# Kernel optimization log

Measured on AMD Instinct MI355X. Metric: run time of the kernel, lower is better.

The kernel has to match this reference:

```python
import jax, jax.numpy as jnp
import numpy as np

B = 1024
E = 512
NUM_HEADS = 8
EPS = 1e-5  # torch LayerNorm default


def _mha(x, w_qkv, b_qkv, w_o, b_o):
    """torch nn.MultiheadAttention (batch_first, self-attn, no dropout).
    x: [N, S, E]; w_qkv: [3E, E]; w_o: [E, E]."""
    N, S, Ex = x.shape
    H = NUM_HEADS
    D = Ex // H
    qkv = x @ w_qkv.T + b_qkv                      # [N, S, 3E]
    q, k, v = jnp.split(qkv, 3, axis=-1)
    q = q.reshape(N, S, H, D).transpose(0, 2, 1, 3)  # [N, H, S, D]
    k = k.reshape(N, S, H, D).transpose(0, 2, 1, 3)
    v = v.reshape(N, S, H, D).transpose(0, 2, 1, 3)
    scores = jnp.einsum('nhqd,nhkd->nhqk', q, k) * (D ** -0.5)
    attn = jax.nn.softmax(scores, axis=-1)
    out = jnp.einsum('nhqk,nhkd->nhqd', attn, v)
    out = out.transpose(0, 2, 1, 3).reshape(N, S, Ex)
    return out @ w_o.T + b_o


def _box_perm(g):
    """Permute 9x9 grid so each 3x3 box becomes a contiguous row of 9.
    This permutation is its own inverse. g: [B, 9, 9, E]."""
    Bx = g.shape[0]
    return (g.reshape(Bx, 3, 3, 3, 3, E)
             .transpose(0, 1, 3, 2, 4, 5)
             .reshape(Bx, 9, 9, E))


def setup_inputs() -> dict:
    key = jax.random.key(0)
    ks = jax.random.split(key, 16)
    s = 0.02
    inp = {'x': jax.random.normal(ks[0], (B, 81, E), jnp.float32)}
    for i, p in enumerate(['row', 'col', 'box']):
        inp[p + '_wqkv'] = jax.random.normal(ks[1 + 2 * i], (3 * E, E), jnp.float32) * s
        inp[p + '_bqkv'] = jnp.zeros((3 * E,), jnp.float32)
        inp[p + '_wo'] = jax.random.normal(ks[2 + 2 * i], (E, E), jnp.float32) * s
        inp[p + '_bo'] = jnp.zeros((E,), jnp.float32)
    inp['w1'] = jax.random.normal(ks[7], (2 * E, 3 * E), jnp.float32) * s
    inp['b1'] = jnp.zeros((2 * E,), jnp.float32)
    inp['w2'] = jax.random.normal(ks[8], (E, 2 * E), jnp.float32) * s
    inp['b2'] = jnp.zeros((E,), jnp.float32)
    inp['gamma'] = jnp.ones((E,), jnp.float32)
    inp['beta'] = jnp.zeros((E,), jnp.float32)
    return inp


def reference(x, row_wqkv, row_bqkv, row_wo, row_bo,
              col_wqkv, col_bqkv, col_wo, col_bo,
              box_wqkv, box_bqkv, box_wo, box_bo,
              w1, b1, w2, b2, gamma, beta):
    Bx = x.shape[0]
    # Row attention: rows are already contiguous groups of 9.
    row_out = _mha(x.reshape(Bx * 9, 9, E), row_wqkv, row_bqkv, row_wo, row_bo)
    row_out = row_out.reshape(Bx, 81, E)
    # Column attention: transpose grid so columns are contiguous.
    col_x = x.reshape(Bx, 9, 9, E).transpose(0, 2, 1, 3).reshape(Bx * 9, 9, E)
    col_out = _mha(col_x, col_wqkv, col_bqkv, col_wo, col_bo)
    col_out = col_out.reshape(Bx, 9, 9, E).transpose(0, 2, 1, 3).reshape(Bx, 81, E)
    # Box attention: permute grid so each 3x3 box is contiguous.
    box_x = _box_perm(x.reshape(Bx, 9, 9, E)).reshape(Bx * 9, 9, E)
    box_out = _mha(box_x, box_wqkv, box_bqkv, box_wo, box_bo)
    box_out = _box_perm(box_out.reshape(Bx, 9, 9, E)).reshape(Bx, 81, E)
    # Constraint mixer MLP.
    combined = jnp.concatenate([row_out, col_out, box_out], axis=-1)  # [B,81,3E]
    h = jax.nn.gelu(combined @ w1.T + b1, approximate=False)
    mixed = h @ w2.T + b2
    # Residual + LayerNorm.
    y = x + mixed
    mu = jnp.mean(y, axis=-1, keepdims=True)
    var = jnp.var(y, axis=-1, keepdims=True)
    return (y - mu) * jax.lax.rsqrt(var + EPS) * gamma + beta
```

## Files before the change

### kernel.cpp

```cpp
#include <hip/hip_runtime.h>
#include <hip/hip_bf16.h>
#include <math.h>

typedef __hip_bfloat16 bf16;
typedef __attribute__((ext_vector_type(8))) short s8v;
typedef __attribute__((ext_vector_type(4))) short s4v;
typedef __attribute__((ext_vector_type(4))) float f4v;

static __device__ __forceinline__ float bfs2f(short s) {
    return __uint_as_float(((unsigned)(unsigned short)s) << 16);
}
static __device__ __forceinline__ short f2bfs(float f) {
    __hip_bfloat16 h = __float2bfloat16(f);
    return *reinterpret_cast<short*>(&h);
}

__global__ __launch_bounds__(256)
void cvt_f32_bf16(const float* __restrict__ in, bf16* __restrict__ out, long n4)
{
    const long i = (long)blockIdx.x * 256 + threadIdx.x;
    if (i >= n4) return;
    const float4 v = reinterpret_cast<const float4*>(in)[i];
    s4v o;
    o[0] = f2bfs(v.x); o[1] = f2bfs(v.y); o[2] = f2bfs(v.z); o[3] = f2bfs(v.w);
    reinterpret_cast<s4v*>(out)[i] = o;
}

__global__ __launch_bounds__(256)
void cvt_t_f32_bf16(const float* __restrict__ in, bf16* __restrict__ out,
                    int R, int C)
{
    __shared__ float t[32][33];
    const int bx = blockIdx.x * 32;
    const int by = blockIdx.y * 32;
    const int tx = threadIdx.x & 31;
    const int ty = threadIdx.x >> 5;
#pragma unroll
    for (int r = ty; r < 32; r += 8)
        t[r][tx] = in[(long)(by + r) * C + bx + tx];
    __syncthreads();
#pragma unroll
    for (int r = ty; r < 32; r += 8)
        out[(long)(bx + r) * R + by + tx] = __float2bfloat16(t[tx][r]);
}

__global__ __launch_bounds__(256)
void fold_b1(const float* __restrict__ w1, const float* __restrict__ bo0,
             const float* __restrict__ bo1, const float* __restrict__ bo2,
             const float* __restrict__ b1, float* __restrict__ b1p)
{
    const int m = blockIdx.x * 256 + threadIdx.x;
    float s = b1[m];
    const float* w = w1 + (long)m * 1536;
    for (int k = 0; k < 512; ++k) s += w[k]        * bo0[k];
    for (int k = 0; k < 512; ++k) s += w[512 + k]  * bo1[k];
    for (int k = 0; k < 512; ++k) s += w[1024 + k] * bo2[k];
    b1p[m] = s;
}

template<int ACT>
__global__ __launch_bounds__(512, 2)
void gemm256(const bf16* __restrict__ A, const bf16* __restrict__ B,
             const float* __restrict__ bias, bf16* __restrict__ C,
             int K, int lda, int ldc, int coff)
{
    __shared__ __align__(16) bf16 sA[2][256 * 64];
    __shared__ __align__(16) bf16 sB[2][256 * 64];
    const int tid  = threadIdx.x;
    const int lane = tid & 63;
    const int wid  = tid >> 6;
    const int nwg  = gridDim.x * gridDim.y;
    const int orig = blockIdx.x + gridDim.x * blockIdx.y;
    const int q = nwg >> 3, r = nwg & 7, xcd = orig & 7;
    const int sb = (xcd < r ? xcd * (q + 1) : r * (q + 1) + (xcd - r) * q) + (orig >> 3);
    const int bCol = sb % gridDim.x;
    const int bRow = sb / gridDim.x;

    const int wr  = (wid >> 2) * 128;
    const int wc  = (wid & 3) * 64;
    const int fr  = lane & 15;
    const int hi4 = lane >> 4;
    const int rx  = fr & 7;

    f4v acc[8][4];
#pragma unroll
    for (int i = 0; i < 8; ++i)
#pragma unroll
        for (int j = 0; j < 4; ++j) acc[i][j] = (f4v)(0.0f);

    const int srow = tid >> 3;
    const int scol = ((tid & 7) ^ (srow & 7)) * 8;
    const bf16* Abase = A + (long)(bRow * 256 + srow) * lda + scol;
    const bf16* Bbase = B + (long)(bCol * 256 + srow) * K + scol;

#define GL16(src, dst)                                                          \
    __builtin_amdgcn_global_load_lds(                                           \
        (const __attribute__((address_space(1))) unsigned int*)(src),           \
        (__attribute__((address_space(3))) unsigned int*)(dst), 16, 0, 0)

#define STAGE_A(h, tt, bc) do {                                                 \
    const bf16* g_ = Abase + (long)(h) * 128 * lda + (long)(tt) * 64;           \
    char* d_ = (char*)sA[bc] + (h) * 16384 + tid * 16;                          \
    GL16(g_, d_); GL16(g_ + 64 * (long)lda, d_ + 8192); } while (0)

#define STAGE_B(h, tt, bc) do {                                                 \
    const bf16* g_ = Bbase + (long)(h) * 128 * K + (long)(tt) * 64;             \
    char* d_ = (char*)sB[bc] + (h) * 16384 + tid * 16;                          \
    GL16(g_, d_); GL16(g_ + 64 * (long)K, d_ + 8192); } while (0)

#define LDSW(base, row, kk)                                                     \
    (*(const s8v*)((base) + (row) * 128 + ((((kk) * 4 + hi4) ^ rx) << 4)))

    const int nk = K >> 6;

    STAGE_A(0, 0, 0); STAGE_A(1, 0, 0);
    STAGE_B(0, 0, 0); STAGE_B(1, 0, 0);
    STAGE_B(0, 1, 1); STAGE_B(1, 1, 1);
    asm volatile("s_waitcnt vmcnt(4)" ::: "memory");
    __builtin_amdgcn_s_barrier();
    __builtin_amdgcn_sched_barrier(0);

    for (int t = 0; t < nk; ++t) {
        const int c = t & 1;
        const char* sAc = (const char*)sA[c];
        const char* sBc = (const char*)sB[c];
        s8v bfr[4][2];

        {
            s8v af0[2][2], af1[2][2];
#pragma unroll
            for (int m2 = 0; m2 < 2; ++m2)
#pragma unroll
                for (int kk = 0; kk < 2; ++kk) {
                    af0[m2][kk] = LDSW(sAc, wr + m2 * 16 + fr, kk);
                    af1[m2][kk] = LDSW(sAc, wr + (2 + m2) * 16 + fr, kk);
                }
#pragma unroll
            for (int ni = 0; ni < 4; ++ni)
#pragma unroll
                for (int kk = 0; kk < 2; ++kk)
                    bfr[ni][kk] = LDSW(sBc, wc + ni * 16 + fr, kk);
            if (t + 1 < nk) { STAGE_A(0, t + 1, c ^ 1); STAGE_A(1, t + 1, c ^ 1); }
            __builtin_amdgcn_s_setprio(1);
#pragma unroll
            for (int kk = 0; kk < 2; ++kk)
#pragma unroll
                for (int m2 = 0; m2 < 2; ++m2)
#pragma unroll
                    for (int ni = 0; ni < 4; ++ni) {
                        acc[m2][ni] = __builtin_amdgcn_mfma_f32_16x16x32_bf16(
                            af0[m2][kk], bfr[ni][kk], acc[m2][ni], 0, 0, 0);
                        acc[2 + m2][ni] = __builtin_amdgcn_mfma_f32_16x16x32_bf16(
                            af1[m2][kk], bfr[ni][kk], acc[2 + m2][ni], 0, 0, 0);
                    }
            __builtin_amdgcn_s_setprio(0);
        }
        __builtin_amdgcn_s_barrier();

        {
            s8v af0[2][2], af1[2][2];
#pragma unroll
            for (int m2 = 0; m2 < 2; ++m2)
#pragma unroll
                for (int kk = 0; kk < 2; ++kk) {
                    af0[m2][kk] = LDSW(sAc, wr + (4 + m2) * 16 + fr, kk);
                    af1[m2][kk] = LDSW(sAc, wr + (6 + m2) * 16 + fr, kk);
                }
            if (t + 2 < nk) { STAGE_B(0, t + 2, c); STAGE_B(1, t + 2, c); }
            __builtin_amdgcn_s_setprio(1);
#pragma unroll
            for (int kk = 0; kk < 2; ++kk)
#pragma unroll
                for (int m2 = 0; m2 < 2; ++m2)
#pragma unroll
                    for (int ni = 0; ni < 4; ++ni) {
                        acc[4 + m2][ni] = __builtin_amdgcn_mfma_f32_16x16x32_bf16(
                            af0[m2][kk], bfr[ni][kk], acc[4 + m2][ni], 0, 0, 0);
                        acc[6 + m2][ni] = __builtin_amdgcn_mfma_f32_16x16x32_bf16(
                            af1[m2][kk], bfr[ni][kk], acc[6 + m2][ni], 0, 0, 0);
                    }
            __builtin_amdgcn_s_setprio(0);
        }
        if (t + 2 < nk) {
            asm volatile("s_waitcnt vmcnt(4)" ::: "memory");
        } else if (t + 1 < nk) {
            asm volatile("s_waitcnt vmcnt(0)" ::: "memory");
        }
        __builtin_amdgcn_s_barrier();
        __builtin_amdgcn_sched_barrier(0);
    }
#undef STAGE_A
#undef STAGE_B
#undef GL16
#undef LDSW

    __syncthreads();
    bf16* ep = (wid < 4) ? ((bf16*)sA + wid * 8192)
                         : ((bf16*)sB + (wid - 4) * 8192);
    const int frow = hi4 * 4;
    const long rowBase = (long)bRow * 256 + wr;
    const int  colBase = bCol * 256 + wc;
#pragma unroll
    for (int ni = 0; ni < 4; ++ni) {
        const int col = colBase + ni * 16 + fr;
        const float bi = bias ? bias[coff + col] : 0.0f;
#pragma unroll
        for (int mi = 0; mi < 8; ++mi) {
#pragma unroll
            for (int j = 0; j < 4; ++j) {
                float v = acc[mi][ni][j] + bi;
                if (ACT == 1) {
                    const float u = v * (0.7978845608f + 0.0356774081f * v * v);
                    const float tnh = 1.0f - 2.0f / (__expf(2.0f * u) + 1.0f);
                    v = 0.5f * v * (1.0f + tnh);
                }
                ep[(mi * 16 + frow + j) * 64 + ni * 16 + fr] = __float2bfloat16(v);
            }
        }
    }
    asm volatile("s_waitcnt lgkmcnt(0)" ::: "memory");
    __builtin_amdgcn_sched_barrier(0);
    const int lr8 = lane >> 3;
    const int lc  = (lane & 7) * 8;
#pragma unroll
    for (int q2 = 0; q2 < 16; ++q2) {
        const int lrow = q2 * 8 + lr8;
        const s8v vv = *(const s8v*)(&ep[lrow * 64 + lc]);
        *(s8v*)(&C[(rowBase + lrow) * (long)ldc + coff + colBase + lc]) = vv;
    }
}

__device__ __forceinline__ int cell9(int branch, int g, int p)
{
    if (branch == 0) return g * 9 + p;
    if (branch == 1) return p * 9 + g;
    return ((g / 3) * 3 + p / 3) * 9 + (g % 3) * 3 + (p % 3);
}

__global__ __launch_bounds__(256)
void attn9(const bf16* __restrict__ qkv, bf16* __restrict__ outg,
           long chunk_base)
{
    __shared__ __align__(16) bf16 sW[4 * 9 * 392];
    __shared__ float sP[4][2][84];
    const int tid  = threadIdx.x;
    const int lane = tid & 63;
    const int w    = tid >> 6;
    const int branch = blockIdx.y;
    const int bx = blockIdx.x;
    const int s = (bx & 7) * (2304 >> 3) + (bx >> 3);
    const int b = s / 9, g = s % 9;
    const long brOff = (long)branch * 1536;
    bf16* myW = sW + w * (9 * 392);

#pragma unroll
    for (int rr = 0; rr < 7; ++rr) {
        const int c = rr * 64 + lane;
        if (c < 432) {
            const int p   = c / 48;
            const int rem = c - p * 48;
            const int seg = rem >> 3;
            const int ch  = rem & 7;
            const int col = (seg >> 1) * 512 + ((w << 1) + (seg & 1)) * 64 + ch * 8;
            const long tok = b * 81 + cell9(branch, g, p);
            *(s8v*)(&myW[p * 392 + seg * 64 + ch * 8]) =
                *(const s8v*)(&qkv[tok * 4608 + brOff + col]);
        }
    }
    asm volatile("s_waitcnt lgkmcnt(0) vmcnt(0)" ::: "memory");
    __builtin_amdgcn_sched_barrier(0);

#pragma unroll
    for (int rr = 0; rr < 3; ++rr) {
        const int idx = rr * 64 + lane;
        if (idx < 162) {
            const int h2 = idx / 81;
            const int pr = idx - h2 * 81;
            const int i = pr / 9, j = pr - (pr / 9) * 9;
            const bf16* qp = &myW[i * 392 + h2 * 64];
            const bf16* kp = &myW[j * 392 + 128 + h2 * 64];
            float accd = 0.0f;
#pragma unroll
            for (int dc = 0; dc < 8; ++dc) {
                s8v qv = *(const s8v*)(qp + dc * 8);
                s8v kv = *(const s8v*)(kp + dc * 8);
#pragma unroll
                for (int e2 = 0; e2 < 8; ++e2)
                    accd += bfs2f(qv[e2]) * bfs2f(kv[e2]);
            }
            sP[w][h2][pr] = accd * 0.125f;
        }
    }
    asm volatile("s_waitcnt lgkmcnt(0)" ::: "memory");
    __builtin_amdgcn_sched_barrier(0);

    if (lane < 18) {
        const int h2 = lane / 9, i = lane - (lane / 9) * 9;
        float* row = &sP[w][h2][i * 9];
        float m = row[0];
#pragma unroll
        for (int j = 1; j < 9; ++j) m = fmaxf(m, row[j]);
        float sum = 0.f, e[9];
#pragma unroll
        for (int j = 0; j < 9; ++j) { e[j] = expf(row[j] - m); sum += e[j]; }
        const float inv = 1.0f / sum;
#pragma unroll
        for (int j = 0; j < 9; ++j) row[j] = e[j] * inv;
    }
    asm volatile("s_waitcnt lgkmcnt(0)" ::: "memory");
    __builtin_amdgcn_sched_barrier(0);

#pragma unroll
    for (int rr = 0; rr < 3; ++rr) {
        const int idx = rr * 64 + lane;
        if (idx < 144) {
            const int h2  = idx / 72;
            const int rem = idx - h2 * 72;
            const int i  = rem >> 3;
            const int c8 = (rem & 7) * 8;
            const float* prow = &sP[w][h2][i * 9];
            float accv[8];
#pragma unroll
            for (int q2 = 0; q2 < 8; ++q2) accv[q2] = 0.f;
#pragma unroll
            for (int j = 0; j < 9; ++j) {
                const float p = prow[j];
                const s8v vv = *(const s8v*)(&myW[j * 392 + 256 + h2 * 64 + c8]);
#pragma unroll
                for (int q2 = 0; q2 < 8; ++q2)
                    accv[q2] += p * bfs2f(vv[q2]);
            }
            s8v ov;
#pragma unroll
            for (int q2 = 0; q2 < 8; ++q2) ov[q2] = f2bfs(accv[q2]);
            const long tok = b * 81 + cell9(branch, g, i);
            const int ocol = ((w << 1) + h2) * 64 + c8;
            *(s8v*)(&outg[(chunk_base + tok) * 1536 + branch * 512 + ocol]) = ov;
        }
    }
}

__global__ __launch_bounds__(256)
void ln_res(const float* __restrict__ x, const bf16* __restrict__ mixed,
            const float* __restrict__ gamma, const float* __restrict__ beta,
            float* __restrict__ out)
{
    const int tid = threadIdx.x;
    const int lane = tid & 63;
    const long row = (long)blockIdx.x * 4 + (tid >> 6);
    const long base = row * 512 + lane * 8;
    const float4 x0 = *(const float4*)(&x[base]);
    const float4 x1 = *(const float4*)(&x[base + 4]);
    const s8v mv = *(const s8v*)(&mixed[base]);
    float y[8];
    y[0] = x0.x + bfs2f(mv[0]); y[1] = x0.y + bfs2f(mv[1]);
    y[2] = x0.z + bfs2f(mv[2]); y[3] = x0.w + bfs2f(mv[3]);
    y[4] = x1.x + bfs2f(mv[4]); y[5] = x1.y + bfs2f(mv[5]);
    y[6] = x1.z + bfs2f(mv[6]); y[7] = x1.w + bfs2f(mv[7]);
    float sum = 0.f, sq = 0.f;
#pragma unroll
    for (int j = 0; j < 8; ++j) { sum += y[j]; sq += y[j] * y[j]; }
#pragma unroll
    for (int o = 32; o > 0; o >>= 1) {
        sum += __shfl_xor(sum, o, 64);
        sq  += __shfl_xor(sq, o, 64);
    }
    const float mean = sum * (1.f / 512.f);
    const float inv = rsqrtf(sq * (1.f / 512.f) - mean * mean + 1e-5f);
    const float4 g0 = *(const float4*)(&gamma[lane * 8]);
    const float4 g1 = *(const float4*)(&gamma[lane * 8 + 4]);
    const float4 b0 = *(const float4*)(&beta[lane * 8]);
    const float4 b1 = *(const float4*)(&beta[lane * 8 + 4]);
    float4 o0, o1;
    o0.x = (y[0] - mean) * inv * g0.x + b0.x;
    o0.y = (y[1] - mean) * inv * g0.y + b0.y;
    o0.z = (y[2] - mean) * inv * g0.z + b0.z;
    o0.w = (y[3] - mean) * inv * g0.w + b0.w;
    o1.x = (y[4] - mean) * inv * g1.x + b1.x;
    o1.y = (y[5] - mean) * inv * g1.y + b1.y;
    o1.z = (y[6] - mean) * inv * g1.z + b1.z;
    o1.w = (y[7] - mean) * inv * g1.w + b1.w;
    *(float4*)(&out[base]) = o0;
    *(float4*)(&out[base + 4]) = o1;
}

extern "C" void kernel_launch(void* const* d_in, const int* in_sizes, int n_in,
                              void* d_out, int out_size, void* d_ws, size_t ws_size,
                              hipStream_t stream)
{
    (void)in_sizes; (void)n_in; (void)out_size; (void)ws_size;
    const float* x     = (const float*)d_in[0];
    const float* w1f   = (const float*)d_in[13];
    const float* b1f   = (const float*)d_in[14];
    const float* b2f   = (const float*)d_in[16];
    const float* gamma = (const float*)d_in[17];
    const float* beta  = (const float*)d_in[18];

    char* ws = (char*)d_ws;
    bf16* attnall   = (bf16*)(ws);
    bf16* mixed     = (bf16*)(ws);
    char* R         = ws + 254803968LL;
    bf16* qkv3chunk = (bf16*)(R);
    bf16* xb        = (bf16*)(R + 191102976LL);
    bf16* h         = (bf16*)(R);
    char* wb        = ws + 530841600LL;
    long off = 0;
    bf16* wqkv3_b = (bf16*)(wb + off); off += 4718592;
    bf16* woT_b[3];
    for (int i = 0; i < 3; ++i) { woT_b[i] = (bf16*)(wb + off); off += 524288; }
    bf16* w1_b  = (bf16*)(wb + off); off += 3145728;
    bf16* w2_b  = (bf16*)(wb + off); off += 1048576;
    bf16* Wp    = (bf16*)(wb + off); off += 3145728;
    float* b1p  = (float*)(wb + off); off += 4096;
    float* bqkv3 = (float*)(wb + off); off += 18432;

    const dim3 blk(256, 1, 1);
    const dim3 blk512(512, 1, 1);

    cvt_f32_bf16<<<dim3(41472), blk, 0, stream>>>(x, xb, 10616832L);
    for (int i = 0; i < 3; ++i) {
        cvt_f32_bf16<<<dim3(768), blk, 0, stream>>>(
            (const float*)d_in[1 + i * 4], wqkv3_b + (long)i * 786432, 196608L);
        cvt_t_f32_bf16<<<dim3(16, 16), blk, 0, stream>>>(
            (const float*)d_in[3 + i * 4], woT_b[i], 512, 512);
        hipMemcpyAsync(bqkv3 + i * 1536, d_in[2 + i * 4], 1536 * sizeof(float),
                       hipMemcpyDeviceToDevice, stream);
    }
    cvt_f32_bf16<<<dim3(1536), blk, 0, stream>>>(w1f, w1_b, 393216L);
    cvt_f32_bf16<<<dim3(512), blk, 0, stream>>>((const float*)d_in[15], w2_b, 131072L);

    fold_b1<<<dim3(4), blk, 0, stream>>>(w1f, (const float*)d_in[4],
                                         (const float*)d_in[8], (const float*)d_in[12],
                                         b1f, b1p);

    for (int br = 0; br < 3; ++br)
        gemm256<0><<<dim3(2, 4), blk512, 0, stream>>>(
            w1_b + br * 512, woT_b[br], nullptr, Wp, 512, 1536, 1536, br * 512);

    const long ROWS_C = 20736;
    for (int c = 0; c < 4; ++c) {
        const bf16* xA = xb + c * ROWS_C * 512;
        gemm256<0><<<dim3(18, 81), blk512, 0, stream>>>(
            xA, wqkv3_b, bqkv3, qkv3chunk, 512, 512, 4608, 0);
        attn9<<<dim3(2304, 3), blk, 0, stream>>>(qkv3chunk, attnall, c * ROWS_C);
    }
    gemm256<1><<<dim3(4, 324), blk512, 0, stream>>>(attnall, Wp, b1p, h, 1536, 1536, 1024, 0);
    gemm256<0><<<dim3(2, 324), blk512, 0, stream>>>(h, w2_b, b2f, mixed, 1024, 1024, 512, 0);
    ln_res<<<dim3(20736), blk, 0, stream>>>(x, mixed, gamma, beta, (float*)d_out);
}
```

Before: 1.425 ms.

## Triple-buffer B tiles in LDS to drop the mid-iteration barrier in gemm256

The B operand in shared memory moves from two buffers to three, indexed by a rotating counter. This lets the prefetch of B two steps ahead go into a buffer nobody is reading, so both the A and B global-to-LDS loads are issued at the top of each iteration and the barrier in the middle of the iteration is removed. The MFMA loop is restructured into four groups of two row-tiles each. LDS use grows from 128 KB to 160 KB per block, which rules out the two blocks per CU the launch bounds ask for and so halves occupancy.

Result: slower. 1.648 ms (+15.7%).

```diff
diff --git a/kernel.cpp b/kernel.cpp
--- a/kernel.cpp
+++ b/kernel.cpp
@@ -65,7 +65,7 @@
              int K, int lda, int ldc, int coff)
 {
     __shared__ __align__(16) bf16 sA[2][256 * 64];
-    __shared__ __align__(16) bf16 sB[2][256 * 64];
+    __shared__ __align__(16) bf16 sB[3][256 * 64];
     const int tid  = threadIdx.x;
     const int lane = tid & 63;
     const int wid  = tid >> 6;
@@ -103,9 +103,9 @@
     char* d_ = (char*)sA[bc] + (h) * 16384 + tid * 16;                          \
     GL16(g_, d_); GL16(g_ + 64 * (long)lda, d_ + 8192); } while (0)
 
-#define STAGE_B(h, tt, bc) do {                                                 \
+#define STAGE_B(h, tt, b3) do {                                                 \
     const bf16* g_ = Bbase + (long)(h) * 128 * K + (long)(tt) * 64;             \
-    char* d_ = (char*)sB[bc] + (h) * 16384 + tid * 16;                          \
+    char* d_ = (char*)sB[b3] + (h) * 16384 + tid * 16;                          \
     GL16(g_, d_); GL16(g_ + 64 * (long)K, d_ + 8192); } while (0)
 
 #define LDSW(base, row, kk)                                                     \
@@ -120,74 +120,54 @@
     __builtin_amdgcn_s_barrier();
     __builtin_amdgcn_sched_barrier(0);
 
+    int cb = 0;
     for (int t = 0; t < nk; ++t) {
-        const int c = t & 1;
-        const char* sAc = (const char*)sA[c];
-        const char* sBc = (const char*)sB[c];
+        const int ca = t & 1;
+        const int wb = (cb == 0) ? 2 : cb - 1;
+        const char* sAc = (const char*)sA[ca];
+        const char* sBc = (const char*)sB[cb];
+
+        if (t + 1 < nk) { STAGE_A(0, t + 1, ca ^ 1); STAGE_A(1, t + 1, ca ^ 1); }
+        if (t + 2 < nk) { STAGE_B(0, t + 2, wb); STAGE_B(1, t + 2, wb); }
+
         s8v bfr[4][2];
-
-        {
-            s8v af0[2][2], af1[2][2];
-#pragma unroll
-            for (int m2 = 0; m2 < 2; ++m2)
-#pragma unroll
-                for (int kk = 0; kk < 2; ++kk) {
-                    af0[m2][kk] = LDSW(sAc, wr + m2 * 16 + fr, kk);
-                    af1[m2][kk] = LDSW(sAc, wr + (2 + m2) * 16 + fr, kk);
+#pragma unroll
+        for (int ni = 0; ni < 4; ++ni)
+#pragma unroll
+            for (int kk = 0; kk < 2; ++kk)
+                bfr[ni][kk] = LDSW(sBc, wc + ni * 16 + fr, kk);
+
+#pragma unroll
+        for (int g = 0; g < 4; ++g) {
+            s8v a0[2], a1[2];
+#pragma unroll
+            for (int kk = 0; kk < 2; ++kk) {
+                a0[kk] = LDSW(sAc, wr + (2 * g) * 16 + fr, kk);
+                a1[kk] = LDSW(sAc, wr + (2 * g + 1) * 16 + fr, kk);
+            }
+            __builtin_amdgcn_s_setprio(1);
+#pragma unroll
+            for (int kk = 0; kk < 2; ++kk)
+#pragma unroll
+                for (int ni = 0; ni < 4; ++ni) {
+                    acc[2 * g][ni] = __builtin_amdgcn_mfma_f32_16x16x32_bf16(
+                        a0[kk], bfr[ni][kk], acc[2 * g][ni], 0, 0, 0);
+                    acc[2 * g + 1][ni] = __builtin_amdgcn_mfma_f32_16x16x32_bf16(
+                        a1[kk], bfr[ni][kk], acc[2 * g + 1][ni], 0, 0, 0);
                 }
-#pragma unroll
-            for (int ni = 0; ni < 4; ++ni)
-#pragma unroll
-                for (int kk = 0; kk < 2; ++kk)
-                    bfr[ni][kk] = LDSW(sBc, wc + ni * 16 + fr, kk);
-            if (t + 1 < nk) { STAGE_A(0, t + 1, c ^ 1); STAGE_A(1, t + 1, c ^ 1); }
-            __builtin_amdgcn_s_setprio(1);
-#pragma unroll
-            for (int kk = 0; kk < 2; ++kk)
-#pragma unroll
-                for (int m2 = 0; m2 < 2; ++m2)
-#pragma unroll
-                    for (int ni = 0; ni < 4; ++ni) {
-                        acc[m2][ni] = __builtin_amdgcn_mfma_f32_16x16x32_bf16(
-                            af0[m2][kk], bfr[ni][kk], acc[m2][ni], 0, 0, 0);
-                        acc[2 + m2][ni] = __builtin_amdgcn_mfma_f32_16x16x32_bf16(
-                            af1[m2][kk], bfr[ni][kk], acc[2 + m2][ni], 0, 0, 0);
-                    }
             __builtin_amdgcn_s_setprio(0);
         }
-        __builtin_amdgcn_s_barrier();
-
-        {
-            s8v af0[2][2], af1[2][2];
-#pragma unroll
-            for (int m2 = 0; m2 < 2; ++m2)
-#pragma unroll
-                for (int kk = 0; kk < 2; ++kk) {
-                    af0[m2][kk] = LDSW(sAc, wr + (4 + m2) * 16 + fr, kk);
-                    af1[m2][kk] = LDSW(sAc, wr + (6 + m2) * 16 + fr, kk);
-                }
-            if (t + 2 < nk) { STAGE_B(0, t + 2, c); STAGE_B(1, t + 2, c); }
-            __builtin_amdgcn_s_setprio(1);
-#pragma unroll
-            for (int kk = 0; kk < 2; ++kk)
-#pragma unroll
-                for (int m2 = 0; m2 < 2; ++m2)
-#pragma unroll
-                    for (int ni = 0; ni < 4; ++ni) {
-                        acc[4 + m2][ni] = __builtin_amdgcn_mfma_f32_16x16x32_bf16(
-                            af0[m2][kk], bfr[ni][kk], acc[4 + m2][ni], 0, 0, 0);
-                        acc[6 + m2][ni] = __builtin_amdgcn_mfma_f32_16x16x32_bf16(
-                            af1[m2][kk], bfr[ni][kk], acc[6 + m2][ni], 0, 0, 0);
-                    }
-            __builtin_amdgcn_s_setprio(0);
-        }
+
         if (t + 2 < nk) {
             asm volatile("s_waitcnt vmcnt(4)" ::: "memory");
+            __builtin_amdgcn_s_barrier();
+            __builtin_amdgcn_sched_barrier(0);
         } else if (t + 1 < nk) {
             asm volatile("s_waitcnt vmcnt(0)" ::: "memory");
-        }
-        __builtin_amdgcn_s_barrier();
-        __builtin_amdgcn_sched_barrier(0);
+            __builtin_amdgcn_s_barrier();
+            __builtin_amdgcn_sched_barrier(0);
+        }
+        cb = (cb == 2) ? 0 : cb + 1;
     }
 #undef STAGE_A
 #undef STAGE_B
```
